# Kernel optimization log

Measured on AMD Instinct MI355X. Metric: run time of the kernel, lower is better.

## Reference

```python
import jax, jax.numpy as jnp
import numpy as np

N, M, E, IN, HID = 100000, 2048, 65536, 512, 256
TAU, LAMDA = 0.5, 1.0


def _l2n(a, eps=1e-12):
    # F.normalize: x / max(||x||_2, eps) along dim=1
    return a / jnp.maximum(jnp.linalg.norm(a, axis=1, keepdims=True), eps)


def setup_inputs() -> dict:
    key = jax.random.key(0)
    ks = jax.random.split(key, 16)
    s = 0.05  # weight scale (xavier-like)
    inp = {
        "x": jax.random.normal(ks[0], (N, IN), jnp.float32),
        "We0": jax.random.normal(ks[1], (IN, HID), jnp.float32) * s,
        "be0": jnp.zeros((HID,), jnp.float32),
        "We1": jax.random.normal(ks[2], (HID, HID), jnp.float32) * s,
        "be1": jnp.zeros((HID,), jnp.float32),
        "Wt0": jax.random.normal(ks[3], (IN, HID), jnp.float32) * s,
        "bt0": jnp.zeros((HID,), jnp.float32),
        "Wt1": jax.random.normal(ks[4], (HID, HID), jnp.float32) * s,
        "bt1": jnp.zeros((HID,), jnp.float32),
        "Wp0": jax.random.normal(ks[5], (HID, HID), jnp.float32) * s,
        "bp0": jnp.zeros((HID,), jnp.float32),
        "Wp1": jax.random.normal(ks[6], (HID, HID), jnp.float32) * s,
        "bp1": jnp.zeros((HID,), jnp.float32),
        "p_vals": jnp.ones((N,), jnp.float32),
        "cg_vals": jax.random.uniform(ks[7], (E,), jnp.float32),
        "p_assign": jax.random.randint(ks[8], (N,), 0, M, jnp.int32),
        "cg_rows": jax.random.randint(ks[9], (E,), 0, M, jnp.int32),
        "cg_cols": jax.random.randint(ks[10], (E,), 0, M, jnp.int32),
        "neg_idx": jax.random.randint(ks[11], (N,), 0, M, jnp.int32),
    }
    return inp


def reference(x, We0, be0, We1, be1, Wt0, bt0, Wt1, bt1,
              Wp0, bp0, Wp1, bp1, p_vals, cg_vals,
              p_assign, cg_rows, cg_cols, neg_idx):
    # encoder: stacked Linears, no activation (batch_norm=layer_norm=False)
    h = (x @ We0 + be0) @ We1 + be1                      # [N, HID]
    # h = spmm(P.T, h): per-cluster weighted sum
    hc = jax.ops.segment_sum(p_vals[:, None] * h, p_assign, num_segments=M)  # [M, HID]
    # target encoder
    v = (x @ Wt0 + bt0) @ Wt1 + bt1                      # [N, HID]

    # pos_score: projector (relu between layers, none on last) + normalize
    q = jax.nn.relu(hc @ Wp0 + bp0) @ Wp1 + bp1          # [M, HID]
    q = _l2n(q)
    vn = _l2n(v)
    pos_sim = jnp.sum(vn * q[p_assign], axis=1) / TAU    # [N]
    pos_score = jnp.exp(
        jax.ops.segment_sum(p_vals * pos_sim, p_assign, num_segments=M))[:, None]  # [M,1]

    # neg_score: dense cluster-cluster similarity
    hn = _l2n(hc)
    neg_score = jnp.exp((hn @ hn.T) / TAU)               # [M, M]

    # partition_score = coarse_g @ neg_score (sparse row-scatter)
    partition_score = jax.ops.segment_sum(
        cg_vals[:, None] * neg_score[cg_cols], cg_rows, num_segments=M)  # [M, M]

    loss = jnp.mean(-jnp.log(pos_score + LAMDA * partition_score)
                    + jnp.log(pos_score + neg_score.sum(axis=1)))
    return loss
```

## Files before the change

kernel.cpp:

```cpp
#include <hip/hip_runtime.h>
#include <hip/hip_bf16.h>
#include <math.h>

#define N_PTS  100000
#define M_CL   2048
#define E_EDG  65536
#define IN_DIM 512
#define HID    256

typedef unsigned short u16;
typedef __attribute__((ext_vector_type(8))) short bf16x8;
typedef __attribute__((ext_vector_type(4))) float f32x4;

__device__ __forceinline__ u16 f2bf(float f){
  __hip_bfloat16 h = __float2bfloat16(f);
  return *reinterpret_cast<u16*>(&h);
}
__device__ __forceinline__ unsigned pk2(float a, float b){
  return (unsigned)f2bf(a) | ((unsigned)f2bf(b) << 16);
}
__device__ __forceinline__ bf16x8 cvt8(f32x4 lo, f32x4 hi){
  bf16x8 r;
  r[0]=(short)f2bf(lo.x); r[1]=(short)f2bf(lo.y); r[2]=(short)f2bf(lo.z); r[3]=(short)f2bf(lo.w);
  r[4]=(short)f2bf(hi.x); r[5]=(short)f2bf(hi.y); r[6]=(short)f2bf(hi.z); r[7]=(short)f2bf(hi.w);
  return r;
}
__device__ __forceinline__ void glds16(const u16* g, u16* l){
  __builtin_amdgcn_global_load_lds(
      (const __attribute__((address_space(1))) unsigned int*)(g),
      (__attribute__((address_space(3))) unsigned int*)(l), 16, 0, 0);
}

static const size_t OFF_POSACC = 0;
static const size_t OFF_NEGSUM = 8192;
static const size_t OFF_HISTP  = 16384;
static const size_t OFF_CURP   = 24576;
static const size_t OFF_HISTE  = 32768;
static const size_t OFF_CURE   = 40960;
static const size_t OFF_LOSS   = 49152;
static const size_t ZERO_BYTES = 49408;
static const size_t OFF_STARTP = 49664;
static const size_t OFF_STARTE = 58112;
static const size_t OFF_SORTPT = 66560;
static const size_t OFF_SCOL   = 466688;
static const size_t OFF_SVAL   = 728832;
static const size_t OFF_CNT    = 990976;
static const size_t OFF_XC     = 999168;
static const size_t OFF_HC     = 5193472;
static const size_t OFF_T0     = 7290624;
static const size_t OFF_Q      = 9387776;
static const size_t OFF_HN     = 11484928;
static const size_t OFF_NEG    = 13582080;
static const size_t OFF_WT0T   = OFF_NEG;
static const size_t OFF_WT1T   = OFF_NEG + 262144;

__global__ __launch_bounds__(256) void k_hist(const int* __restrict__ idx, int n, int* __restrict__ hist){
  int i = blockIdx.x*256 + threadIdx.x;
  if (i < n) atomicAdd(&hist[idx[i]], 1);
}

__global__ __launch_bounds__(256) void k_scan(const int* __restrict__ hist, int* __restrict__ start){
  __shared__ int part[256];
  int t = threadIdx.x;
  int v[8]; int s = 0;
#pragma unroll
  for (int j=0;j<8;j++){ v[j] = hist[t*8+j]; s += v[j]; }
  part[t] = s;
  __syncthreads();
  if (t == 0){
    int run = 0;
    for (int i=0;i<256;i++){ int tmp = part[i]; part[i] = run; run += tmp; }
  }
  __syncthreads();
  int run = part[t];
#pragma unroll
  for (int j=0;j<8;j++){ start[t*8+j] = run; run += v[j]; }
  if (t == 255) start[M_CL] = run;
}

__global__ __launch_bounds__(256) void k_scatter_pts(const int* __restrict__ assign, const int* __restrict__ start,
                                                     int* __restrict__ cur, int* __restrict__ out){
  int i = blockIdx.x*256 + threadIdx.x;
  if (i < N_PTS){
    int r = assign[i];
    int p = start[r] + atomicAdd(&cur[r], 1);
    out[p] = i;
  }
}

__global__ __launch_bounds__(256) void k_scatter_edges(const int* __restrict__ rows, const int* __restrict__ cols,
                                                       const float* __restrict__ vals, const int* __restrict__ start,
                                                       int* __restrict__ cur, int* __restrict__ scol,
                                                       float* __restrict__ sval){
  int e = blockIdx.x*256 + threadIdx.x;
  if (e < E_EDG){
    int r = rows[e];
    int p = start[r] + atomicAdd(&cur[r], 1);
    scol[p] = cols[e];
    sval[p] = vals[e];
  }
}

__global__ __launch_bounds__(256) void k_cluster_agg(const float* __restrict__ x, const float* __restrict__ pv,
                                                     const int* __restrict__ sorted_pt, const int* __restrict__ start,
                                                     float* __restrict__ Xc, float* __restrict__ cnt){
  int m = blockIdx.x, t = threadIdx.x;
  int s0 = start[m], s1 = start[m+1];
  float a0 = 0.f, a1 = 0.f, c = 0.f;
  for (int p=s0;p<s1;p++){
    int row = sorted_pt[p];
    float w = pv[row];
    float2 xv = *reinterpret_cast<const float2*>(x + (size_t)row*IN_DIM + t*2);
    a0 = fmaf(w, xv.x, a0);
    a1 = fmaf(w, xv.y, a1);
    c += w;
  }
  *reinterpret_cast<float2*>(Xc + (size_t)m*IN_DIM + t*2) = make_float2(a0, a1);
  if (t == 0) cnt[m] = c;
}

template<int K, int ROWS, bool RELU, bool SCALED>
__global__ __launch_bounds__(256) void k_gemm_small(const float* __restrict__ A, const float* __restrict__ W,
                                                    const float* __restrict__ bias, const float* __restrict__ scale,
                                                    float* __restrict__ out){
  __shared__ __align__(16) float a_sh[ROWS][K];
  int rb = blockIdx.x*ROWS, t = threadIdx.x;
  for (int i=t; i<ROWS*(K/4); i+=256){
    int r = i/(K/4), k4 = i%(K/4);
    reinterpret_cast<float4*>(a_sh[r])[k4] = reinterpret_cast<const float4*>(A + (size_t)(rb+r)*K)[k4];
  }
  __syncthreads();
  float acc[ROWS];
#pragma unroll
  for (int r=0;r<ROWS;r++) acc[r] = 0.f;
#pragma unroll 2
  for (int k=0;k<K;k+=4){
    float w0 = W[(size_t)(k+0)*HID + t];
    float w1 = W[(size_t)(k+1)*HID + t];
    float w2 = W[(size_t)(k+2)*HID + t];
    float w3 = W[(size_t)(k+3)*HID + t];
#pragma unroll
    for (int r=0;r<ROWS;r++){
      float4 av = *reinterpret_cast<const float4*>(&a_sh[r][k]);
      acc[r] = fmaf(av.x, w0, acc[r]);
      acc[r] = fmaf(av.y, w1, acc[r]);
      acc[r] = fmaf(av.z, w2, acc[r]);
      acc[r] = fmaf(av.w, w3, acc[r]);
    }
  }
  float b = bias[t];
#pragma unroll
  for (int r=0;r<ROWS;r++){
    float s = SCALED ? scale[rb+r] : 1.0f;
    float v = acc[r] + s*b;
    if (RELU) v = fmaxf(v, 0.0f);
    out[(size_t)(rb+r)*HID + t] = v;
  }
}

__global__ __launch_bounds__(256) void k_norm_rows(const float* __restrict__ in, float* __restrict__ out){
  int r = blockIdx.x, t = threadIdx.x;
  float v = in[(size_t)r*HID + t];
  float ss = v*v;
#pragma unroll
  for (int off=32;off;off>>=1) ss += __shfl_xor(ss, off, 64);
  __shared__ float wsum[4];
  if ((t&63) == 0) wsum[t>>6] = ss;
  __syncthreads();
  float tot = wsum[0]+wsum[1]+wsum[2]+wsum[3];
  float inv = 1.0f / fmaxf(sqrtf(tot), 1e-12f);
  out[(size_t)r*HID + t] = v*inv;
}

template<int K>
__global__ __launch_bounds__(256) void k_transpose_bf16(const float* __restrict__ W, u16* __restrict__ Wt){
  int o = blockIdx.x*256 + threadIdx.x;
  int n = o / K, k = o % K;
  Wt[o] = f2bf(W[(size_t)k*HID + n]);
}

__global__ __launch_bounds__(256,2) void k_target_mfma(
    const float* __restrict__ x, const u16* __restrict__ Wt0t, const float* __restrict__ bt0,
    const u16* __restrict__ Wt1t, const float* __restrict__ bt1,
    const float* __restrict__ q, const int* __restrict__ assign,
    const float* __restrict__ pv, float* __restrict__ posacc){
  __shared__ u16 ws[2*8192];
  __shared__ u16 act[16384];
  __shared__ float red[2][4][4][16];
  u16* xs = act;

  const int t  = threadIdx.x;
  const int w  = t >> 6;
  const int l  = t & 63;
  const int c  = l & 15;
  const int lg = l >> 4;
  const int gm0 = blockIdx.x * 64;

  const int s_row = t >> 2;
  const int s_u   = t & 3;
  const int sx_g  = gm0 + s_row;
  const float* xsrc = x + (size_t)((sx_g < N_PTS) ? sx_g : (N_PTS-1))*IN_DIM + s_u*8;
  const int sx_off = (s_row*4 + (s_u ^ ((s_row>>1)&3)))*8;

  f32x4 acc[4][4];
#pragma unroll
  for (int i=0;i<4;i++)
#pragma unroll
    for (int j=0;j<4;j++){ acc[i][j].x=0.f; acc[i][j].y=0.f; acc[i][j].z=0.f; acc[i][j].w=0.f; }

  #define STAGE_W(Wt, K, k0, buf) do { \
    _Pragma("unroll") \
    for (int i_=0;i_<4;i_++){ \
      int row_ = w*64 + i_*16 + (l>>2); \
      int ug_  = (l&3) ^ ((row_>>1)&3); \
      glds16((Wt) + (size_t)row_*(K) + (k0) + ug_*8, \
             ws + (buf)*8192 + (w*64 + i_*16)*32 + l*8); \
    } } while(0)

  #define STAGE_X(k0, buf) do { \
    f32x4 a_ = *reinterpret_cast<const f32x4*>(xsrc + (k0)); \
    f32x4 b_ = *reinterpret_cast<const f32x4*>(xsrc + (k0) + 4); \
    *reinterpret_cast<bf16x8*>(xs + (buf)*2048 + sx_off) = cvt8(a_, b_); \
  } while(0)

  const int su = lg ^ ((c>>1)&3);

  STAGE_W(Wt0t, IN_DIM, 0, 0);
  STAGE_X(0, 0);
  __syncthreads();
#pragma unroll
  for (int ks=0; ks<16; ks++){
    int buf = ks & 1;
    if (ks < 15){ STAGE_W(Wt0t, IN_DIM, (ks+1)*32, buf^1); STAGE_X((ks+1)*32, buf^1); }
    bf16x8 bfr[4];
#pragma unroll
    for (int mf=0; mf<4; mf++)
      bfr[mf] = *reinterpret_cast<const bf16x8*>(xs + buf*2048 + ((mf*16+c)*4 + su)*8);
#pragma unroll
    for (int nf=0; nf<4; nf++){
      bf16x8 afr = *reinterpret_cast<const bf16x8*>(ws + buf*8192 + ((w*64+nf*16+c)*4 + su)*8);
#pragma unroll
      for (int mf=0; mf<4; mf++)
        acc[mf][nf] = __builtin_amdgcn_mfma_f32_16x16x32_bf16(afr, bfr[mf], acc[mf][nf], 0,0,0);
    }
    __syncthreads();
  }

#pragma unroll
  for (int nf=0; nf<4; nf++){
    f32x4 bias = *reinterpret_cast<const f32x4*>(bt0 + w*64 + nf*16 + lg*4);
#pragma unroll
    for (int mf=0; mf<4; mf++){
      int m = mf*16 + c;
      f32x4 v = acc[mf][nf] + bias;
      uint2 p; p.x = pk2(v.x, v.y); p.y = pk2(v.z, v.w);
      int u = (w*8 + nf*2 + (lg>>1)) ^ (c&7);
      *reinterpret_cast<uint2*>(act + (m*32 + u)*8 + (lg&1)*4) = p;
    }
  }
#pragma unroll
  for (int i=0;i<4;i++)
#pragma unroll
    for (int j=0;j<4;j++){ acc[i][j].x=0.f; acc[i][j].y=0.f; acc[i][j].z=0.f; acc[i][j].w=0.f; }
  STAGE_W(Wt1t, HID, 0, 0);
  __syncthreads();

#pragma unroll
  for (int ks=0; ks<8; ks++){
    int buf = ks & 1;
    if (ks < 7) STAGE_W(Wt1t, HID, (ks+1)*32, buf^1);
    bf16x8 bfr[4];
#pragma unroll
    for (int mf=0; mf<4; mf++){
      int m = mf*16 + c;
      int u = (ks*4 + lg) ^ (c&7);
      bfr[mf] = *reinterpret_cast<const bf16x8*>(act + (m*32 + u)*8);
    }
#pragma unroll
    for (int nf=0; nf<4; nf++){
      bf16x8 afr = *reinterpret_cast<const bf16x8*>(ws + buf*8192 + ((w*64+nf*16+c)*4 + su)*8);
#pragma unroll
      for (int mf=0; mf<4; mf++)
        acc[mf][nf] = __builtin_amdgcn_mfma_f32_16x16x32_bf16(afr, bfr[mf], acc[mf][nf], 0,0,0);
    }
    __syncthreads();
  }

#pragma unroll
  for (int mf=0; mf<4; mf++){
    int gm = gm0 + mf*16 + c;
    int cl = assign[(gm < N_PTS) ? gm : (N_PTS-1)];
    const float* qrow = q + (size_t)cl*HID + w*64 + lg*4;
    float ss = 0.f, d = 0.f;
#pragma unroll
    for (int nf=0; nf<4; nf++){
      f32x4 b  = *reinterpret_cast<const f32x4*>(bt1 + w*64 + nf*16 + lg*4);
      f32x4 qv = *reinterpret_cast<const f32x4*>(qrow + nf*16);
      f32x4 v  = acc[mf][nf] + b;
      ss = fmaf(v.x,v.x, fmaf(v.y,v.y, fmaf(v.z,v.z, fmaf(v.w,v.w, ss))));
      d  = fmaf(v.x,qv.x, fmaf(v.y,qv.y, fmaf(v.z,qv.z, fmaf(v.w,qv.w, d))));
    }
    ss += __shfl_xor(ss, 16, 64); ss += __shfl_xor(ss, 32, 64);
    d  += __shfl_xor(d , 16, 64); d  += __shfl_xor(d , 32, 64);
    if (lg == 0){ red[0][w][mf][c] = ss; red[1][w][mf][c] = d; }
  }
  __syncthreads();
  if (t < 64){
    int gm = gm0 + t;
    if (gm < N_PTS){
      int mf = t>>4, cc = t&15;
      float ss = red[0][0][mf][cc]+red[0][1][mf][cc]+red[0][2][mf][cc]+red[0][3][mf][cc];
      float d  = red[1][0][mf][cc]+red[1][1][mf][cc]+red[1][2][mf][cc]+red[1][3][mf][cc];
      float inv = 1.0f / fmaxf(sqrtf(ss), 1e-12f);
      atomicAdd(&posacc[assign[gm]], pv[gm] * d * inv * 2.0f);
    }
  }
  #undef STAGE_W
  #undef STAGE_X
}

__global__ __launch_bounds__(256) void k_neg(const float* __restrict__ hn, float* __restrict__ neg,
                                             float* __restrict__ negsum){
  __shared__ __align__(16) float at[64*64];
  __shared__ __align__(16) float bt[64*64];
  const int t  = threadIdx.x;
  const int ty = t >> 4, tx = t & 15;
  const int i0 = blockIdx.y*64, j0 = blockIdx.x*64;
  const int r  = t & 63, kq = t >> 6;
  float acc[4][4] = {};
  for (int kc=0;kc<4;kc++){
    int k0 = kc*64;
    float4 av[4], bv[4];
#pragma unroll
    for (int j=0;j<4;j++){
      int kb = kq*16 + j*4;
      av[j] = *reinterpret_cast<const float4*>(hn + (size_t)(i0+r)*HID + k0 + kb);
      bv[j] = *reinterpret_cast<const float4*>(hn + (size_t)(j0+r)*HID + k0 + kb);
    }
    __syncthreads();
#pragma unroll
    for (int j=0;j<4;j++){
      int kb = kq*16 + j*4;
      at[(kb+0)*64+r]=av[j].x; at[(kb+1)*64+r]=av[j].y; at[(kb+2)*64+r]=av[j].z; at[(kb+3)*64+r]=av[j].w;
      bt[(kb+0)*64+r]=bv[j].x; bt[(kb+1)*64+r]=bv[j].y; bt[(kb+2)*64+r]=bv[j].z; bt[(kb+3)*64+r]=bv[j].w;
    }
    __syncthreads();
#pragma unroll 8
    for (int k=0;k<64;k++){
      float4 a = *reinterpret_cast<const float4*>(&at[k*64 + ty*4]);
      float4 b = *reinterpret_cast<const float4*>(&bt[k*64 + tx*4]);
      float aa[4] = {a.x,a.y,a.z,a.w}, bb[4] = {b.x,b.y,b.z,b.w};
#pragma unroll
      for (int ii=0;ii<4;ii++)
#pragma unroll
        for (int jj=0;jj<4;jj++) acc[ii][jj] = fmaf(aa[ii], bb[jj], acc[ii][jj]);
    }
  }
#pragma unroll
  for (int ii=0;ii<4;ii++){
    float4 e;
    e.x = __expf(acc[ii][0]*2.0f);
    e.y = __expf(acc[ii][1]*2.0f);
    e.z = __expf(acc[ii][2]*2.0f);
    e.w = __expf(acc[ii][3]*2.0f);
    int row = i0 + ty*4 + ii;
    *reinterpret_cast<float4*>(neg + (size_t)row*M_CL + j0 + tx*4) = e;
    float rs = e.x+e.y+e.z+e.w;
#pragma unroll
    for (int off=8;off;off>>=1) rs += __shfl_xor(rs, off, 16);
    if (tx == 0) atomicAdd(&negsum[row], rs);
  }
}

__global__ __launch_bounds__(256) void k_loss(const float* __restrict__ neg, const float* __restrict__ negsum,
                                              const float* __restrict__ posacc, const int* __restrict__ start,
                                              const int* __restrict__ scol, const float* __restrict__ sval,
                                              double* __restrict__ loss){
  const int i = blockIdx.x, t = threadIdx.x;
  float ps[8] = {};
  const int s0 = start[i], s1 = start[i+1];
  for (int e=s0;e<s1;e++){
    int c = scol[e];
    float v = sval[e];
    const float* row = neg + (size_t)c*M_CL + t;
#pragma unroll
    for (int jj=0;jj<8;jj++) ps[jj] = fmaf(v, row[jj*256], ps[jj]);
  }
  float pos = __expf(posacc[i]);
  float part = 0.f;
#pragma unroll
  for (int jj=0;jj<8;jj++){
    int j = t + jj*256;
    part += __logf(pos + negsum[j]) - __logf(pos + ps[jj]);
  }
#pragma unroll
  for (int off=32;off;off>>=1) part += __shfl_xor(part, off, 64);
  __shared__ float wsum[4];
  if ((t&63) == 0) wsum[t>>6] = part;
  __syncthreads();
  if (t == 0){
    double s = (double)wsum[0] + (double)wsum[1] + (double)wsum[2] + (double)wsum[3];
    atomicAdd(loss, s);
  }
}

__global__ void k_finalize(const double* __restrict__ loss, float* __restrict__ out){
  if (threadIdx.x == 0 && blockIdx.x == 0)
    out[0] = (float)(loss[0] / ((double)M_CL * (double)M_CL));
}

extern "C" void kernel_launch(void* const* d_in, const int* in_sizes, int n_in,
                              void* d_out, int out_size, void* d_ws, size_t ws_size,
                              hipStream_t stream){
  const float* x    = (const float*)d_in[0];
  const float* We0  = (const float*)d_in[1];
  const float* be0  = (const float*)d_in[2];
  const float* We1  = (const float*)d_in[3];
  const float* be1  = (const float*)d_in[4];
  const float* Wt0  = (const float*)d_in[5];
  const float* bt0  = (const float*)d_in[6];
  const float* Wt1  = (const float*)d_in[7];
  const float* bt1  = (const float*)d_in[8];
  const float* Wp0  = (const float*)d_in[9];
  const float* bp0  = (const float*)d_in[10];
  const float* Wp1  = (const float*)d_in[11];
  const float* bp1  = (const float*)d_in[12];
  const float* pv   = (const float*)d_in[13];
  const float* cgv  = (const float*)d_in[14];
  const int*   pas  = (const int*)d_in[15];
  const int*   cgr  = (const int*)d_in[16];
  const int*   cgc  = (const int*)d_in[17];

  char* ws = (char*)d_ws;
  float*  posacc  = (float*)(ws + OFF_POSACC);
  float*  negsum  = (float*)(ws + OFF_NEGSUM);
  int*    hist_p  = (int*)  (ws + OFF_HISTP);
  int*    cur_p   = (int*)  (ws + OFF_CURP);
  int*    hist_e  = (int*)  (ws + OFF_HISTE);
  int*    cur_e   = (int*)  (ws + OFF_CURE);
  double* lossd   = (double*)(ws + OFF_LOSS);
  int*    start_p = (int*)  (ws + OFF_STARTP);
  int*    start_e = (int*)  (ws + OFF_STARTE);
  int*    sortpt  = (int*)  (ws + OFF_SORTPT);
  int*    scol    = (int*)  (ws + OFF_SCOL);
  float*  sval    = (float*)(ws + OFF_SVAL);
  float*  cnt     = (float*)(ws + OFF_CNT);
  float*  Xc      = (float*)(ws + OFF_XC);
  float*  hc      = (float*)(ws + OFF_HC);
  float*  t0      = (float*)(ws + OFF_T0);
  float*  qb      = (float*)(ws + OFF_Q);
  float*  hn      = (float*)(ws + OFF_HN);
  float*  negbuf  = (float*)(ws + OFF_NEG);
  u16*    Wt0t    = (u16*)  (ws + OFF_WT0T);
  u16*    Wt1t    = (u16*)  (ws + OFF_WT1T);

  hipMemsetAsync(ws, 0, ZERO_BYTES, stream);

  k_hist<<<(N_PTS+255)/256, 256, 0, stream>>>(pas, N_PTS, hist_p);
  k_hist<<<(E_EDG+255)/256, 256, 0, stream>>>(cgr, E_EDG, hist_e);
  k_scan<<<1, 256, 0, stream>>>(hist_p, start_p);
  k_scan<<<1, 256, 0, stream>>>(hist_e, start_e);
  k_scatter_pts<<<(N_PTS+255)/256, 256, 0, stream>>>(pas, start_p, cur_p, sortpt);
  k_scatter_edges<<<(E_EDG+255)/256, 256, 0, stream>>>(cgr, cgc, cgv, start_e, cur_e, scol, sval);

  k_transpose_bf16<IN_DIM><<<IN_DIM, 256, 0, stream>>>(Wt0, Wt0t);
  k_transpose_bf16<HID  ><<<HID,    256, 0, stream>>>(Wt1, Wt1t);

  k_cluster_agg<<<M_CL, 256, 0, stream>>>(x, pv, sortpt, start_p, Xc, cnt);

  k_gemm_small<512,8,false,true ><<<M_CL/8, 256, 0, stream>>>(Xc, We0, be0, cnt, t0);
  k_gemm_small<256,8,false,true ><<<M_CL/8, 256, 0, stream>>>(t0, We1, be1, cnt, hc);
  k_gemm_small<256,8,true ,false><<<M_CL/8, 256, 0, stream>>>(hc, Wp0, bp0, nullptr, t0);
  k_gemm_small<256,8,false,false><<<M_CL/8, 256, 0, stream>>>(t0, Wp1, bp1, nullptr, qb);

  k_norm_rows<<<M_CL, 256, 0, stream>>>(qb, qb);
  k_norm_rows<<<M_CL, 256, 0, stream>>>(hc, hn);

  k_target_mfma<<<(N_PTS+63)/64, 256, 0, stream>>>(x, Wt0t, bt0, Wt1t, bt1, qb, pas, pv, posacc);

  dim3 g2(M_CL/64, M_CL/64);
  k_neg<<<g2, 256, 0, stream>>>(hn, negbuf, negsum);

  k_loss<<<M_CL, 256, 0, stream>>>(negbuf, negsum, posacc, start_e, scol, sval, lossd);
  k_finalize<<<1, 64, 0, stream>>>(lossd, (float*)d_out);
}
```

Before: 377.8 us.

## Fuse cluster MLP chain, emit bf16 x, and move neg similarity to MFMA

Four fp32 small GEMM kernels and two row-normalisation kernels are merged into one per-cluster chain kernel that writes a bf16 normalised hc and the normalised q. The cluster aggregation pass now also writes a bf16 copy of x, so the target-encoder MFMA kernel can stage x with direct global-to-LDS loads instead of converting fp32 in registers. The dense cluster-cluster similarity moves from an fp32 FMA kernel to a bf16 MFMA kernel, and the exp(neg) matrix is stored as bf16 so the loss kernel reads half the bytes. The trade-offs are lower precision in the neg matrix, an extra 100MB bf16 write of x, and fewer blocks in the fused chain kernel.

```diff
diff --git a/kernel.cpp b/kernel.cpp
--- a/kernel.cpp
+++ b/kernel.cpp
@@ -19,11 +19,8 @@
 __device__ __forceinline__ unsigned pk2(float a, float b){
   return (unsigned)f2bf(a) | ((unsigned)f2bf(b) << 16);
 }
-__device__ __forceinline__ bf16x8 cvt8(f32x4 lo, f32x4 hi){
-  bf16x8 r;
-  r[0]=(short)f2bf(lo.x); r[1]=(short)f2bf(lo.y); r[2]=(short)f2bf(lo.z); r[3]=(short)f2bf(lo.w);
-  r[4]=(short)f2bf(hi.x); r[5]=(short)f2bf(hi.y); r[6]=(short)f2bf(hi.z); r[7]=(short)f2bf(hi.w);
-  return r;
+__device__ __forceinline__ float bf2f(u16 v){
+  return __uint_as_float((unsigned)v << 16);
 }
 __device__ __forceinline__ void glds16(const u16* g, u16* l){
   __builtin_amdgcn_global_load_lds(
@@ -46,13 +43,12 @@
 static const size_t OFF_SVAL   = 728832;
 static const size_t OFF_CNT    = 990976;
 static const size_t OFF_XC     = 999168;
-static const size_t OFF_HC     = 5193472;
-static const size_t OFF_T0     = 7290624;
 static const size_t OFF_Q      = 9387776;
-static const size_t OFF_HN     = 11484928;
-static const size_t OFF_NEG    = 13582080;
-static const size_t OFF_WT0T   = OFF_NEG;
-static const size_t OFF_WT1T   = OFF_NEG + 262144;
+static const size_t OFF_HNB    = 11484928;
+static const size_t OFF_NEGB   = 13582080;
+static const size_t OFF_WT0T   = 22020096;
+static const size_t OFF_WT1T   = 22282240;
+static const size_t OFF_XBF    = 33554432;
 
 __global__ __launch_bounds__(256) void k_hist(const int* __restrict__ idx, int n, int* __restrict__ hist){
   int i = blockIdx.x*256 + threadIdx.x;
@@ -103,7 +99,8 @@
 
 __global__ __launch_bounds__(256) void k_cluster_agg(const float* __restrict__ x, const float* __restrict__ pv,
                                                      const int* __restrict__ sorted_pt, const int* __restrict__ start,
-                                                     float* __restrict__ Xc, float* __restrict__ cnt){
+                                                     float* __restrict__ Xc, float* __restrict__ cnt,
+                                                     u16* __restrict__ xbf){
   int m = blockIdx.x, t = threadIdx.x;
   int s0 = start[m], s1 = start[m+1];
   float a0 = 0.f, a1 = 0.f, c = 0.f;
@@ -114,25 +111,23 @@
     a0 = fmaf(w, xv.x, a0);
     a1 = fmaf(w, xv.y, a1);
     c += w;
+    *reinterpret_cast<unsigned*>(xbf + (size_t)row*IN_DIM + t*2) = pk2(xv.x, xv.y);
   }
   *reinterpret_cast<float2*>(Xc + (size_t)m*IN_DIM + t*2) = make_float2(a0, a1);
   if (t == 0) cnt[m] = c;
 }
 
-template<int K, int ROWS, bool RELU, bool SCALED>
-__global__ __launch_bounds__(256) void k_gemm_small(const float* __restrict__ A, const float* __restrict__ W,
-                                                    const float* __restrict__ bias, const float* __restrict__ scale,
-                                                    float* __restrict__ out){
-  __shared__ __align__(16) float a_sh[ROWS][K];
-  int rb = blockIdx.x*ROWS, t = threadIdx.x;
-  for (int i=t; i<ROWS*(K/4); i+=256){
-    int r = i/(K/4), k4 = i%(K/4);
-    reinterpret_cast<float4*>(a_sh[r])[k4] = reinterpret_cast<const float4*>(A + (size_t)(rb+r)*K)[k4];
-  }
-  __syncthreads();
-  float acc[ROWS];
-#pragma unroll
-  for (int r=0;r<ROWS;r++) acc[r] = 0.f;
+template<int K>
+__global__ __launch_bounds__(256) void k_transpose_bf16(const float* __restrict__ W, u16* __restrict__ Wt){
+  int o = blockIdx.x*256 + threadIdx.x;
+  int n = o / K, k = o % K;
+  Wt[o] = f2bf(W[(size_t)k*HID + n]);
+}
+
+template<int K>
+__device__ __forceinline__ void mc_layer(const float* __restrict__ W, const float* act, int t, float acc[4]){
+#pragma unroll
+  for (int r=0;r<4;r++) acc[r] = 0.f;
 #pragma unroll 2
   for (int k=0;k<K;k+=4){
     float w0 = W[(size_t)(k+0)*HID + t];
@@ -140,47 +135,96 @@
     float w2 = W[(size_t)(k+2)*HID + t];
     float w3 = W[(size_t)(k+3)*HID + t];
 #pragma unroll
-    for (int r=0;r<ROWS;r++){
-      float4 av = *reinterpret_cast<const float4*>(&a_sh[r][k]);
+    for (int r=0;r<4;r++){
+      float4 av = *reinterpret_cast<const float4*>(act + r*K + k);
       acc[r] = fmaf(av.x, w0, acc[r]);
       acc[r] = fmaf(av.y, w1, acc[r]);
       acc[r] = fmaf(av.z, w2, acc[r]);
       acc[r] = fmaf(av.w, w3, acc[r]);
     }
   }
-  float b = bias[t];
-#pragma unroll
-  for (int r=0;r<ROWS;r++){
-    float s = SCALED ? scale[rb+r] : 1.0f;
-    float v = acc[r] + s*b;
-    if (RELU) v = fmaxf(v, 0.0f);
-    out[(size_t)(rb+r)*HID + t] = v;
-  }
-}
-
-__global__ __launch_bounds__(256) void k_norm_rows(const float* __restrict__ in, float* __restrict__ out){
-  int r = blockIdx.x, t = threadIdx.x;
-  float v = in[(size_t)r*HID + t];
-  float ss = v*v;
-#pragma unroll
-  for (int off=32;off;off>>=1) ss += __shfl_xor(ss, off, 64);
-  __shared__ float wsum[4];
-  if ((t&63) == 0) wsum[t>>6] = ss;
-  __syncthreads();
-  float tot = wsum[0]+wsum[1]+wsum[2]+wsum[3];
-  float inv = 1.0f / fmaxf(sqrtf(tot), 1e-12f);
-  out[(size_t)r*HID + t] = v*inv;
-}
-
-template<int K>
-__global__ __launch_bounds__(256) void k_transpose_bf16(const float* __restrict__ W, u16* __restrict__ Wt){
-  int o = blockIdx.x*256 + threadIdx.x;
-  int n = o / K, k = o % K;
-  Wt[o] = f2bf(W[(size_t)k*HID + n]);
+}
+
+__global__ __launch_bounds__(256) void k_mchain(
+    const float* __restrict__ Xc, const float* __restrict__ cnt,
+    const float* __restrict__ We0, const float* __restrict__ be0,
+    const float* __restrict__ We1, const float* __restrict__ be1,
+    const float* __restrict__ Wp0, const float* __restrict__ bp0,
+    const float* __restrict__ Wp1, const float* __restrict__ bp1,
+    u16* __restrict__ hnb, float* __restrict__ q){
+  __shared__ __align__(16) float a_sh[4*512];
+  __shared__ __align__(16) float b_sh[4*256];
+  __shared__ float part[4][4];
+  const int t = threadIdx.x;
+  const int rb = blockIdx.x*4;
+  for (int i=t; i<4*128; i+=256){
+    int r = i>>7, k4 = i&127;
+    reinterpret_cast<float4*>(a_sh + r*512)[k4] =
+      reinterpret_cast<const float4*>(Xc + (size_t)(rb+r)*IN_DIM)[k4];
+  }
+  float cv[4];
+#pragma unroll
+  for (int r=0;r<4;r++) cv[r] = cnt[rb+r];
+  __syncthreads();
+
+  float acc[4], v[4];
+  mc_layer<512>(We0, a_sh, t, acc);
+  {
+    float b = be0[t];
+#pragma unroll
+    for (int r=0;r<4;r++) b_sh[r*256+t] = fmaf(cv[r], b, acc[r]);
+  }
+  __syncthreads();
+  mc_layer<256>(We1, b_sh, t, acc);
+  {
+    float b = be1[t];
+#pragma unroll
+    for (int r=0;r<4;r++){
+      v[r] = fmaf(cv[r], b, acc[r]);
+      float s = v[r]*v[r];
+#pragma unroll
+      for (int off=32;off;off>>=1) s += __shfl_xor(s, off, 64);
+      if ((t&63) == 0) part[t>>6][r] = s;
+      a_sh[r*256+t] = v[r];
+    }
+  }
+  __syncthreads();
+#pragma unroll
+  for (int r=0;r<4;r++){
+    float tot = part[0][r]+part[1][r]+part[2][r]+part[3][r];
+    float inv = 1.0f / fmaxf(sqrtf(tot), 1e-12f);
+    hnb[(size_t)(rb+r)*HID + t] = f2bf(v[r]*inv);
+  }
+  mc_layer<256>(Wp0, a_sh, t, acc);
+  {
+    float b = bp0[t];
+#pragma unroll
+    for (int r=0;r<4;r++) b_sh[r*256+t] = fmaxf(acc[r]+b, 0.f);
+  }
+  __syncthreads();
+  mc_layer<256>(Wp1, b_sh, t, acc);
+  {
+    float b = bp1[t];
+#pragma unroll
+    for (int r=0;r<4;r++){
+      v[r] = acc[r] + b;
+      float s = v[r]*v[r];
+#pragma unroll
+      for (int off=32;off;off>>=1) s += __shfl_xor(s, off, 64);
+      if ((t&63) == 0) part[t>>6][r] = s;
+    }
+  }
+  __syncthreads();
+#pragma unroll
+  for (int r=0;r<4;r++){
+    float tot = part[0][r]+part[1][r]+part[2][r]+part[3][r];
+    float inv = 1.0f / fmaxf(sqrtf(tot), 1e-12f);
+    q[(size_t)(rb+r)*HID + t] = v[r]*inv;
+  }
 }
 
 __global__ __launch_bounds__(256,2) void k_target_mfma(
-    const float* __restrict__ x, const u16* __restrict__ Wt0t, const float* __restrict__ bt0,
+    const u16* __restrict__ xbf, const u16* __restrict__ Wt0t, const float* __restrict__ bt0,
     const u16* __restrict__ Wt1t, const float* __restrict__ bt1,
     const float* __restrict__ q, const int* __restrict__ assign,
     const float* __restrict__ pv, float* __restrict__ posacc){
@@ -196,11 +240,10 @@
   const int lg = l >> 4;
   const int gm0 = blockIdx.x * 64;
 
-  const int s_row = t >> 2;
-  const int s_u   = t & 3;
-  const int sx_g  = gm0 + s_row;
-  const float* xsrc = x + (size_t)((sx_g < N_PTS) ? sx_g : (N_PTS-1))*IN_DIM + s_u*8;
-  const int sx_off = (s_row*4 + (s_u ^ ((s_row>>1)&3)))*8;
+  const int sxr = w*16 + (l>>2);
+  int sxg = gm0 + sxr; if (sxg >= N_PTS) sxg = N_PTS-1;
+  const u16* xsrc = xbf + (size_t)sxg*IN_DIM + ((l&3) ^ ((sxr>>1)&3))*8;
+  u16* xdst = xs + (w*64 + l)*8;
 
   f32x4 acc[4][4];
 #pragma unroll
@@ -216,12 +259,7 @@
       glds16((Wt) + (size_t)row_*(K) + (k0) + ug_*8, \
              ws + (buf)*8192 + (w*64 + i_*16)*32 + l*8); \
     } } while(0)
-
-  #define STAGE_X(k0, buf) do { \
-    f32x4 a_ = *reinterpret_cast<const f32x4*>(xsrc + (k0)); \
-    f32x4 b_ = *reinterpret_cast<const f32x4*>(xsrc + (k0) + 4); \
-    *reinterpret_cast<bf16x8*>(xs + (buf)*2048 + sx_off) = cvt8(a_, b_); \
-  } while(0)
+  #define STAGE_X(k0, buf) glds16(xsrc + (k0), xdst + (buf)*2048)
 
   const int su = lg ^ ((c>>1)&3);
 
@@ -319,60 +357,81 @@
   #undef STAGE_X
 }
 
-__global__ __launch_bounds__(256) void k_neg(const float* __restrict__ hn, float* __restrict__ neg,
-                                             float* __restrict__ negsum){
-  __shared__ __align__(16) float at[64*64];
-  __shared__ __align__(16) float bt[64*64];
+__global__ __launch_bounds__(256,2) void k_neg_mfma(
+    const u16* __restrict__ hnb, u16* __restrict__ negb, float* __restrict__ negsum){
+  __shared__ u16 wsb[2*8192];
+  __shared__ u16 xsb[2*2048];
   const int t  = threadIdx.x;
-  const int ty = t >> 4, tx = t & 15;
-  const int i0 = blockIdx.y*64, j0 = blockIdx.x*64;
-  const int r  = t & 63, kq = t >> 6;
-  float acc[4][4] = {};
-  for (int kc=0;kc<4;kc++){
-    int k0 = kc*64;
-    float4 av[4], bv[4];
-#pragma unroll
-    for (int j=0;j<4;j++){
-      int kb = kq*16 + j*4;
-      av[j] = *reinterpret_cast<const float4*>(hn + (size_t)(i0+r)*HID + k0 + kb);
-      bv[j] = *reinterpret_cast<const float4*>(hn + (size_t)(j0+r)*HID + k0 + kb);
+  const int w  = t >> 6;
+  const int l  = t & 63;
+  const int c  = l & 15;
+  const int lg = l >> 4;
+  const int j0 = blockIdx.x * 256;
+  const int i0 = blockIdx.y * 64;
+
+  const int sxr = w*16 + (l>>2);
+  const u16* xsrc = hnb + (size_t)(i0+sxr)*HID + ((l&3) ^ ((sxr>>1)&3))*8;
+  u16* xdst = xsb + (w*64 + l)*8;
+
+  f32x4 acc[4][4];
+#pragma unroll
+  for (int i=0;i<4;i++)
+#pragma unroll
+    for (int j=0;j<4;j++){ acc[i][j].x=0.f; acc[i][j].y=0.f; acc[i][j].z=0.f; acc[i][j].w=0.f; }
+
+  #define NSTAGE_W(k0, buf) do { \
+    _Pragma("unroll") \
+    for (int i_=0;i_<4;i_++){ \
+      int row_ = w*64 + i_*16 + (l>>2); \
+      int ug_  = (l&3) ^ ((row_>>1)&3); \
+      glds16(hnb + (size_t)(j0+row_)*HID + (k0) + ug_*8, \
+             wsb + (buf)*8192 + (w*64 + i_*16)*32 + l*8); \
+    } } while(0)
+  #define NSTAGE_X(k0, buf) glds16(xsrc + (k0), xdst + (buf)*2048)
+
+  NSTAGE_W(0, 0);
+  NSTAGE_X(0, 0);
+  __syncthreads();
+  const int su = lg ^ ((c>>1)&3);
+#pragma unroll
+  for (int ks=0; ks<8; ks++){
+    int buf = ks & 1;
+    if (ks < 7){ NSTAGE_W((ks+1)*32, buf^1); NSTAGE_X((ks+1)*32, buf^1); }
+    bf16x8 bfr[4];
+#pragma unroll
+    for (int mf=0; mf<4; mf++)
+      bfr[mf] = *reinterpret_cast<const bf16x8*>(xsb + buf*2048 + ((mf*16+c)*4 + su)*8);
+#pragma unroll
+    for (int nf=0; nf<4; nf++){
+      bf16x8 afr = *reinterpret_cast<const bf16x8*>(wsb + buf*8192 + ((w*64+nf*16+c)*4 + su)*8);
+#pragma unroll
+      for (int mf=0; mf<4; mf++)
+        acc[mf][nf] = __builtin_amdgcn_mfma_f32_16x16x32_bf16(afr, bfr[mf], acc[mf][nf], 0,0,0);
     }
     __syncthreads();
-#pragma unroll
-    for (int j=0;j<4;j++){
-      int kb = kq*16 + j*4;
-      at[(kb+0)*64+r]=av[j].x; at[(kb+1)*64+r]=av[j].y; at[(kb+2)*64+r]=av[j].z; at[(kb+3)*64+r]=av[j].w;
-      bt[(kb+0)*64+r]=bv[j].x; bt[(kb+1)*64+r]=bv[j].y; bt[(kb+2)*64+r]=bv[j].z; bt[(kb+3)*64+r]=bv[j].w;
-    }
-    __syncthreads();
-#pragma unroll 8
-    for (int k=0;k<64;k++){
-      float4 a = *reinterpret_cast<const float4*>(&at[k*64 + ty*4]);
-      float4 b = *reinterpret_cast<const float4*>(&bt[k*64 + tx*4]);
-      float aa[4] = {a.x,a.y,a.z,a.w}, bb[4] = {b.x,b.y,b.z,b.w};
-#pragma unroll
-      for (int ii=0;ii<4;ii++)
-#pragma unroll
-        for (int jj=0;jj<4;jj++) acc[ii][jj] = fmaf(aa[ii], bb[jj], acc[ii][jj]);
-    }
-  }
-#pragma unroll
-  for (int ii=0;ii<4;ii++){
-    float4 e;
-    e.x = __expf(acc[ii][0]*2.0f);
-    e.y = __expf(acc[ii][1]*2.0f);
-    e.z = __expf(acc[ii][2]*2.0f);
-    e.w = __expf(acc[ii][3]*2.0f);
-    int row = i0 + ty*4 + ii;
-    *reinterpret_cast<float4*>(neg + (size_t)row*M_CL + j0 + tx*4) = e;
-    float rs = e.x+e.y+e.z+e.w;
-#pragma unroll
-    for (int off=8;off;off>>=1) rs += __shfl_xor(rs, off, 16);
-    if (tx == 0) atomicAdd(&negsum[row], rs);
-  }
-}
-
-__global__ __launch_bounds__(256) void k_loss(const float* __restrict__ neg, const float* __restrict__ negsum,
+  }
+
+#pragma unroll
+  for (int mf=0; mf<4; mf++){
+    int i = i0 + mf*16 + c;
+    float rs = 0.f;
+#pragma unroll
+    for (int nf=0; nf<4; nf++){
+      f32x4 a = acc[mf][nf];
+      float e0 = __expf(a.x*2.0f), e1 = __expf(a.y*2.0f);
+      float e2 = __expf(a.z*2.0f), e3 = __expf(a.w*2.0f);
+      rs += e0+e1+e2+e3;
+      uint2 p; p.x = pk2(e0, e1); p.y = pk2(e2, e3);
+      *reinterpret_cast<uint2*>(negb + (size_t)i*M_CL + j0 + w*64 + nf*16 + lg*4) = p;
+    }
+    rs += __shfl_xor(rs, 16, 64); rs += __shfl_xor(rs, 32, 64);
+    if (lg == 0) atomicAdd(&negsum[i], rs);
+  }
+  #undef NSTAGE_W
+  #undef NSTAGE_X
+}
+
+__global__ __launch_bounds__(256) void k_loss(const u16* __restrict__ negb, const float* __restrict__ negsum,
                                               const float* __restrict__ posacc, const int* __restrict__ start,
                                               const int* __restrict__ scol, const float* __restrict__ sval,
                                               double* __restrict__ loss){
@@ -382,9 +441,9 @@
   for (int e=s0;e<s1;e++){
     int c = scol[e];
     float v = sval[e];
-    const float* row = neg + (size_t)c*M_CL + t;
-#pragma unroll
-    for (int jj=0;jj<8;jj++) ps[jj] = fmaf(v, row[jj*256], ps[jj]);
+    const u16* row = negb + (size_t)c*M_CL + t;
+#pragma unroll
+    for (int jj=0;jj<8;jj++) ps[jj] = fmaf(v, bf2f(row[jj*256]), ps[jj]);
   }
   float pos = __expf(posacc[i]);
   float part = 0.f;
@@ -446,13 +505,12 @@
   float*  sval    = (float*)(ws + OFF_SVAL);
   float*  cnt     = (float*)(ws + OFF_CNT);
   float*  Xc      = (float*)(ws + OFF_XC);
-  float*  hc      = (float*)(ws + OFF_HC);
-  float*  t0      = (float*)(ws + OFF_T0);
   float*  qb      = (float*)(ws + OFF_Q);
-  float*  hn      = (float*)(ws + OFF_HN);
-  float*  negbuf  = (float*)(ws + OFF_NEG);
+  u16*    hnb     = (u16*)  (ws + OFF_HNB);
+  u16*    negb    = (u16*)  (ws + OFF_NEGB);
   u16*    Wt0t    = (u16*)  (ws + OFF_WT0T);
   u16*    Wt1t    = (u16*)  (ws + OFF_WT1T);
+  u16*    xbf     = (u16*)  (ws + OFF_XBF);
 
   hipMemsetAsync(ws, 0, ZERO_BYTES, stream);
 
@@ -466,21 +524,15 @@
   k_transpose_bf16<IN_DIM><<<IN_DIM, 256, 0, stream>>>(Wt0, Wt0t);
   k_transpose_bf16<HID  ><<<HID,    256, 0, stream>>>(Wt1, Wt1t);
 
-  k_cluster_agg<<<M_CL, 256, 0, stream>>>(x, pv, sortpt, start_p, Xc, cnt);
-
-  k_gemm_small<512,8,false,true ><<<M_CL/8, 256, 0, stream>>>(Xc, We0, be0, cnt, t0);
-  k_gemm_small<256,8,false,true ><<<M_CL/8, 256, 0, stream>>>(t0, We1, be1, cnt, hc);
-  k_gemm_small<256,8,true ,false><<<M_CL/8, 256, 0, stream>>>(hc, Wp0, bp0, nullptr, t0);
-  k_gemm_small<256,8,false,false><<<M_CL/8, 256, 0, stream>>>(t0, Wp1, bp1, nullptr, qb);
-
-  k_norm_rows<<<M_CL, 256, 0, stream>>>(qb, qb);
-  k_norm_rows<<<M_CL, 256, 0, stream>>>(hc, hn);
-
-  k_target_mfma<<<(N_PTS+63)/64, 256, 0, stream>>>(x, Wt0t, bt0, Wt1t, bt1, qb, pas, pv, posacc);
-
-  dim3 g2(M_CL/64, M_CL/64);
-  k_neg<<<g2, 256, 0, stream>>>(hn, negbuf, negsum);
-
-  k_loss<<<M_CL, 256, 0, stream>>>(negbuf, negsum, posacc, start_e, scol, sval, lossd);
+  k_cluster_agg<<<M_CL, 256, 0, stream>>>(x, pv, sortpt, start_p, Xc, cnt, xbf);
+
+  k_mchain<<<M_CL/4, 256, 0, stream>>>(Xc, cnt, We0, be0, We1, be1, Wp0, bp0, Wp1, bp1, hnb, qb);
+
+  k_target_mfma<<<(N_PTS+63)/64, 256, 0, stream>>>(xbf, Wt0t, bt0, Wt1t, bt1, qb, pas, pv, posacc);
+
+  dim3 gneg(M_CL/256, M_CL/64);
+  k_neg_mfma<<<gneg, 256, 0, stream>>>(hnb, negb, negsum);
+
+  k_loss<<<M_CL, 256, 0, stream>>>(negb, negsum, posacc, start_e, scol, sval, lossd);
   k_finalize<<<1, 64, 0, stream>>>(lossd, (float*)d_out);
 }
```

Result: faster. 350.4 us (-7.2%).
